# Kernel tuning notes

Hardware: AMD Instinct MI355X
Metric: run time of the kernel (lower is better)

The kernel has to match this reference:

```python
import jax, jax.numpy as jnp
import numpy as np

SHIFTS = [1, 3, 5, 7]
C = 16  # in_channels // 4
# -1 neighbor offsets for tmp1..tmp8 (dy, dx) in units of the dilation
OFFSETS = [(-1, -1), (-1, 0), (-1, 1), (0, 1), (1, 1), (1, 0), (1, -1), (0, -1)]


def setup_inputs() -> dict:
    key = jax.random.key(0)
    ks = jax.random.split(key, 32)
    d = {}
    d['cen'] = jax.random.normal(ks[0], (8, 64, 256, 256), jnp.float32)
    d['mas'] = jax.random.normal(ks[1], (8, 1, 256, 256), jnp.float32)
    d['in_conv_w'] = jax.random.normal(ks[2], (16, 64), jnp.float32) * 0.1
    d['in_conv_b'] = jax.random.normal(ks[3], (16,), jnp.float32) * 0.1
    for i, s in enumerate(SHIFTS):
        d[f'dw_w{s}'] = jax.random.normal(ks[4 + 2 * i], (16, 1, s, s), jnp.float32) * 0.1
        d[f'dw_b{s}'] = jax.random.normal(ks[5 + 2 * i], (16,), jnp.float32) * 0.1
    d['l1_w'] = jax.random.normal(ks[12], (4, 16, 4), jnp.float32) * 0.1
    d['l1_b'] = jax.random.normal(ks[13], (4, 16), jnp.float32) * 0.1
    d['l2_w'] = jax.random.normal(ks[14], (4, 16, 8), jnp.float32) * 0.1
    d['l2_b'] = jax.random.normal(ks[15], (4, 16), jnp.float32) * 0.1
    d['base_w'] = jax.random.normal(ks[16], (16, 4), jnp.float32) * 0.1
    d['bn_scale'] = jnp.ones((16,), jnp.float32)
    d['bn_bias'] = jnp.zeros((16,), jnp.float32)
    d['final_w'] = jax.random.normal(ks[17], (1, 16), jnp.float32) * 0.1
    d['final_b'] = jax.random.normal(ks[18], (1,), jnp.float32) * 0.1
    return d


def _dw_conv(x, w, b, pad):
    # depthwise conv, groups == channels
    y = jax.lax.conv_general_dilated(
        x, w, window_strides=(1, 1), padding=[(pad, pad), (pad, pad)],
        dimension_numbers=('NCHW', 'OIHW', 'NCHW'), feature_group_count=x.shape[1])
    return y + b[None, :, None, None]


def _shifted(x, dy, dx, d):
    # zero-padded shift: out(y,x) = in(y+dy, x+dx)
    H, W = x.shape[2], x.shape[3]
    p = jnp.pad(x, ((0, 0), (0, 0), (d, d), (d, d)))
    return p[:, :, d + dy:d + dy + H, d + dx:d + dx + W]


def _circ_shift(x, dw_w, dw_b, w1, b1, w2, b2, shift):
    x = _dw_conv(x, dw_w, dw_b, shift // 2)
    # tmp_k = x - x shifted by the k-th neighbor offset (dilation = shift)
    T = [x - _shifted(x, dy * shift, dx * shift, shift) for dy, dx in OFFSETS]
    # paired sums: S[k] = tmp_{k+1} + tmp_{k+5} (S repeats with period 4)
    S = [T[k] + T[k + 4] for k in range(4)]
    outs = []
    for k in range(8):  # fixed small structural loop
        feats = jnp.stack([S[(k + 1) % 4], S[(k + 3) % 4], S[(k + 2) % 4],
                           2.0 * T[(k + 4) % 8]], axis=2)  # (B,C,4,H,W)
        # grouped 1x1 conv (groups=C, 4C->C) == per-channel contraction over feature axis
        o = jnp.einsum('bcfhw,cf->bchw', feats, w1) + b1[None, :, None, None]
        outs.append(o * T[k])
    O = jnp.sort(jnp.stack(outs, axis=2), axis=2)  # (B,C,8,H,W) sorted over branch axis
    return jnp.einsum('bcfhw,cf->bchw', O, w2) + b2[None, :, None, None]


def reference(cen, mas, in_conv_w, in_conv_b, dw_w1, dw_b1, dw_w3, dw_b3,
              dw_w5, dw_b5, dw_w7, dw_b7, l1_w, l1_b, l2_w, l2_b,
              base_w, bn_scale, bn_bias, final_w, final_b):
    # in_conv: 1x1, in_channels -> C
    x = jnp.einsum('bihw,oi->bohw', cen, in_conv_w) + in_conv_b[None, :, None, None]
    dws = [(dw_w1, dw_b1), (dw_w3, dw_b3), (dw_w5, dw_b5), (dw_w7, dw_b7)]
    branches = [
        _circ_shift(x, dws[i][0], dws[i][1], l1_w[i], l1_b[i], l2_w[i], l2_b[i], SHIFTS[i])
        for i in range(len(SHIFTS))
    ]
    A = jnp.sort(jnp.stack(branches, axis=2), axis=2)  # (B,C,4,H,W)
    # out_conv: grouped 1x1 BaseConv (conv no-bias + BN(affine) + SiLU), then 1x1 -> 1, sigmoid
    y = jnp.einsum('bcfhw,cf->bchw', A, base_w)
    y = jax.nn.silu(y * bn_scale[None, :, None, None] + bn_bias[None, :, None, None])
    y = jnp.einsum('bchw,oc->bohw', y, final_w) + final_b[None, :, None, None]
    return jax.nn.sigmoid(y)
```

## Files before the change

kernel.cpp:

```cpp
#include <hip/hip_runtime.h>
#include <hip/hip_fp16.h>
#include <math.h>

#define HW 65536
#define PITCH 272
#define PLANE (PITCH * PITCH)

typedef float v2f __attribute__((ext_vector_type(2), aligned(8)));
typedef _Float16 h2 __attribute__((ext_vector_type(2)));

__device__ __forceinline__ h2 uh(unsigned u) { return __builtin_bit_cast(h2, u); }

#define CEH(a, b) { h2 _t = __builtin_elementwise_min(a, b); \
                    b = __builtin_elementwise_max(a, b); a = _t; }

__device__ __forceinline__ void sort8_h2(h2* v) {
    CEH(v[0], v[1]); CEH(v[2], v[3]); CEH(v[4], v[5]); CEH(v[6], v[7]);
    CEH(v[0], v[2]); CEH(v[1], v[3]); CEH(v[4], v[6]); CEH(v[5], v[7]);
    CEH(v[1], v[2]); CEH(v[5], v[6]); CEH(v[0], v[4]); CEH(v[3], v[7]);
    CEH(v[1], v[5]); CEH(v[2], v[6]);
    CEH(v[1], v[4]); CEH(v[3], v[6]);
    CEH(v[2], v[4]); CEH(v[3], v[5]);
    CEH(v[3], v[4]);
}
__device__ __forceinline__ void sort4_h2(h2* v) {
    CEH(v[0], v[1]); CEH(v[2], v[3]); CEH(v[0], v[2]); CEH(v[1], v[3]); CEH(v[1], v[2]);
}

__global__ __launch_bounds__(256) void k_pack(const float* __restrict__ l1w,
                                              const float* __restrict__ l1b,
                                              const float* __restrict__ l2w,
                                              const float* __restrict__ l2b,
                                              const float* __restrict__ bw,
                                              unsigned* __restrict__ wtab) {
    for (int t = threadIdx.x; t < 1088; t += 256) {
        float v = 0.f;
        if (t < 1024) {
            int c = t >> 6, i = (t >> 4) & 3, j = t & 15;
            if (j < 3)        v = l1w[i * 64 + c * 4 + j];
            else if (j == 3)  v = 2.f * l1w[i * 64 + c * 4 + 3];
            else if (j == 4)  v = l1b[i * 16 + c];
            else if (j < 13)  v = l2w[i * 128 + c * 8 + (j - 5)];
            else if (j == 13) v = l2b[i * 16 + c];
        } else {
            v = bw[t - 1024];
        }
        unsigned hs = (unsigned)__half_as_ushort(__float2half(v));
        wtab[t] = hs * 0x10001u;
    }
}

__global__ __launch_bounds__(256, 4) void k_inconv(const float* __restrict__ cen,
                                                   const float* __restrict__ w,
                                                   const float* __restrict__ bias,
                                                   __half* __restrict__ xh) {
    __shared__ float wl[1040];
    int tid = threadIdx.x;
    for (int t = tid; t < 1024; t += 256) wl[t] = w[(t & 15) * 64 + (t >> 4)];
    if (tid < 16) wl[1024 + tid] = bias[tid];
    __syncthreads();

    int q  = blockIdx.x * 256 + tid;
    int b_ = q >> 14;
    int hw = (q & 16383) * 4;
    const float* src = cen + (size_t)(b_ * 64) * HW + hw;

    float4 acc[16];
#pragma unroll
    for (int o = 0; o < 16; o++) { float bv = wl[1024 + o]; acc[o] = make_float4(bv, bv, bv, bv); }

#pragma unroll 4
    for (int i = 0; i < 64; i++) {
        float4 xv = *(const float4*)(src + (size_t)i * HW);
        const float4* wq = (const float4*)&wl[i * 16];
#pragma unroll
        for (int g = 0; g < 4; g++) {
            float4 f = wq[g];
            acc[g * 4 + 0].x += xv.x * f.x; acc[g * 4 + 0].y += xv.y * f.x;
            acc[g * 4 + 0].z += xv.z * f.x; acc[g * 4 + 0].w += xv.w * f.x;
            acc[g * 4 + 1].x += xv.x * f.y; acc[g * 4 + 1].y += xv.y * f.y;
            acc[g * 4 + 1].z += xv.z * f.y; acc[g * 4 + 1].w += xv.w * f.y;
            acc[g * 4 + 2].x += xv.x * f.z; acc[g * 4 + 2].y += xv.y * f.z;
            acc[g * 4 + 2].z += xv.z * f.z; acc[g * 4 + 2].w += xv.w * f.z;
            acc[g * 4 + 3].x += xv.x * f.w; acc[g * 4 + 3].y += xv.y * f.w;
            acc[g * 4 + 3].z += xv.z * f.w; acc[g * 4 + 3].w += xv.w * f.w;
        }
    }
    __half* dst = xh + (size_t)(b_ * 16) * HW + hw;
#pragma unroll
    for (int o = 0; o < 16; o++) {
        uint2 pk;
        pk.x = __builtin_bit_cast(unsigned, __floats2half2_rn(acc[o].x, acc[o].y));
        pk.y = __builtin_bit_cast(unsigned, __floats2half2_rn(acc[o].z, acc[o].w));
        *(uint2*)(dst + (size_t)o * HW) = pk;
    }
}

__global__ __launch_bounds__(256) void k_dw(const __half* __restrict__ xh,
    const float* __restrict__ dw_w1, const float* __restrict__ dw_b1,
    const float* __restrict__ dw_w3, const float* __restrict__ dw_b3,
    const float* __restrict__ dw_w5, const float* __restrict__ dw_b5,
    const float* __restrict__ dw_w7, const float* __restrict__ dw_b7,
    __half* __restrict__ conv) {
    const int plane = blockIdx.y;
    const int c     = plane & 15;
    const int P0    = (blockIdx.x >> 3) * 34;
    const int Q0    = (blockIdx.x & 7) * 34;
    const int tid   = threadIdx.x;

    __shared__ float lx[40 * 44];
    const __half* xp = xh + (size_t)plane * HW;

    for (int t = tid; t < 40 * 21; t += 256) {
        int r = t / 21, d = t - r * 21;
        int gy = P0 - 10 + r, gx = Q0 - 10 + 2 * d;
        float2 v = make_float2(0.f, 0.f);
        if ((unsigned)gy < 256u && (unsigned)gx < 256u)
            v = __half22float2(*(const __half2*)(xp + gy * 256 + gx));
        lx[r * 44 + 2 * d]     = v.x;
        lx[r * 44 + 2 * d + 1] = v.y;
    }
    __syncthreads();

    const float* W7 = dw_w7 + c * 49;
    const float* W5 = dw_w5 + c * 25;
    const float* W3 = dw_w3 + c * 9;
    const float  W1 = dw_w1[c];
    const float  B1 = dw_b1[c], B3 = dw_b3[c], B5 = dw_b5[c], B7 = dw_b7[c];

    for (int u = tid; u < 34 * 17; u += 256) {
        int row = u / 17;
        int pc0 = (u - row * 17) * 2;
        v2f c7v = {0, 0}, c5v = {0, 0}, c3v = {0, 0}, c1v = {0, 0};
#pragma unroll
        for (int a = 0; a < 7; a++) {
            const float* rp = &lx[(row + a) * 44 + pc0];
            v2f q0 = *(const v2f*)rp;
            v2f q1 = *(const v2f*)(rp + 2);
            v2f q2 = *(const v2f*)(rp + 4);
            v2f q3 = *(const v2f*)(rp + 6);
            float v8 = rp[8];
            float v[9] = {q0.x, q0.y, q1.x, q1.y, q2.x, q2.y, q3.x, q3.y, v8};
#pragma unroll
            for (int bb = 0; bb < 7; bb++) {
                v2f vv = {v[bb], v[bb + 1]};
                c7v += vv * W7[a * 7 + bb];
            }
            if (a >= 1 && a <= 5) {
#pragma unroll
                for (int bb = 0; bb < 5; bb++) {
                    v2f vv = {v[bb + 1], v[bb + 2]};
                    c5v += vv * W5[(a - 1) * 5 + bb];
                }
            }
            if (a >= 2 && a <= 4) {
#pragma unroll
                for (int bb = 0; bb < 3; bb++) {
                    v2f vv = {v[bb + 2], v[bb + 3]};
                    c3v += vv * W3[(a - 2) * 3 + bb];
                }
            }
            if (a == 3) {
                v2f vv = {v[3], v[4]};
                c1v = vv * W1;
            }
        }
        int py = P0 + row, px = Q0 + pc0;
        int iy = py - 7, ix = px - 7;
        bool rin = (unsigned)iy < 256u;
        bool in0 = rin && (unsigned)ix < 256u;
        bool in1 = rin && (unsigned)(ix + 1) < 256u;
        size_t o = (size_t)(plane * 4) * PLANE + (size_t)py * PITCH + px;
        *(__half2*)&conv[o]             = __floats2half2_rn(in0 ? c1v.x + B1 : 0.f, in1 ? c1v.y + B1 : 0.f);
        *(__half2*)&conv[o + PLANE]     = __floats2half2_rn(in0 ? c3v.x + B3 : 0.f, in1 ? c3v.y + B3 : 0.f);
        *(__half2*)&conv[o + 2 * PLANE] = __floats2half2_rn(in0 ? c5v.x + B5 : 0.f, in1 ? c5v.y + B5 : 0.f);
        *(__half2*)&conv[o + 3 * PLANE] = __floats2half2_rn(in0 ? c7v.x + B7 : 0.f, in1 ? c7v.y + B7 : 0.f);
    }
}

__global__ __launch_bounds__(512, 4) void k_mach(const __half* __restrict__ conv,
                                                 const unsigned* __restrict__ wtab,
                                                 const float* __restrict__ bns,
                                                 const float* __restrict__ bnb,
                                                 const float* __restrict__ fw,
                                                 const float* __restrict__ fb,
                                                 float* __restrict__ out) {
    const int b_  = blockIdx.y;
    const int ty0 = (blockIdx.x >> 3) * 32;
    const int tx0 = (blockIdx.x & 7) * 32;
    const int tid = threadIdx.x;
    const int py  = tid >> 4;
    const int pxp = tid & 15;

    __shared__ __align__(16) unsigned convt[4 * 46 * 24];

    float fyx = fb[0], fyy = fb[0];

    for (int c = 0; c < 16; c++) {
        if (c) __syncthreads();
        {
            const size_t pb4 = (size_t)(b_ * 64 + c * 4) * PLANE;
#pragma unroll
            for (int j = 0; j < 5; j++) {
                int t = tid + j * 512;
                if (t < 2208) {
                    int i  = t / 552;
                    int rm = t - i * 552;
                    int r  = rm / 12;
                    int d2 = rm - r * 12;
                    size_t E = pb4 + (size_t)i * PLANE + (size_t)(ty0 + r) * PITCH + tx0 + 4 * d2;
                    ((uint2*)convt)[t] = *(const uint2*)(conv + E);
                }
            }
        }
        __syncthreads();

        h2 bh[4];
#pragma unroll
        for (int i = 0; i < 4; i++) {
            const int s = 1 + 2 * i;
            const unsigned* pl = convt + i * 1104;
            const int q    = pxp + (7 - s) / 2;
            const int topb = (py + 7 - s) * 24 + q;
            const int midb = (py + 7) * 24 + q;
            const int botb = (py + 7 + s) * 24 + q;

            unsigned tt[8], tm[8], tb[8];
#pragma unroll
            for (int k = 0; k <= s; k++) {
                tt[k] = pl[topb + k];
                tm[k] = pl[midb + k];
                tb[k] = pl[botb + k];
            }
            const int m = s >> 1;
            h2 n0  = uh(tt[0]);
            h2 n1  = uh((tt[m] >> 16) | (tt[m + 1] << 16));
            h2 n2  = uh(tt[s]);
            h2 n7  = uh(tm[0]);
            h2 ctr = uh((tm[m] >> 16) | (tm[m + 1] << 16));
            h2 n3  = uh(tm[s]);
            h2 n6  = uh(tb[0]);
            h2 n5  = uh((tb[m] >> 16) | (tb[m + 1] << 16));
            h2 n4  = uh(tb[s]);

            h2 T[8];
            T[0] = ctr - n0; T[1] = ctr - n1; T[2] = ctr - n2; T[3] = ctr - n3;
            T[4] = ctr - n4; T[5] = ctr - n5; T[6] = ctr - n6; T[7] = ctr - n7;
            h2 S[4];
#pragma unroll
            for (int k = 0; k < 4; k++) S[k] = T[k] + T[k + 4];

            const unsigned* wt = wtab + ((c << 2) + i) * 16;
            h2 w10 = uh(wt[0]), w11 = uh(wt[1]), w12 = uh(wt[2]);
            h2 w13x2 = uh(wt[3]), bb1 = uh(wt[4]);

            h2 R[4];
#pragma unroll
            for (int mm = 0; mm < 4; mm++) {
                h2 r = S[(mm + 2) & 3] * w12 + bb1;
                r = S[(mm + 3) & 3] * w11 + r;
                r = S[(mm + 1) & 3] * w10 + r;
                R[mm] = r;
            }
            h2 h8[8];
#pragma unroll
            for (int k = 0; k < 8; k++)
                h8[k] = (T[(k + 4) & 7] * w13x2 + R[k & 3]) * T[k];
            sort8_h2(h8);

            h2 acc = uh(wt[13]);
#pragma unroll
            for (int k = 0; k < 8; k++) acc += h8[k] * uh(wt[5 + k]);
            bh[i] = acc;
        }
        sort4_h2(bh);
        h2 yv = bh[0] * uh(wtab[1024 + (c << 2)]);
#pragma unroll
        for (int k = 1; k < 4; k++) yv = bh[k] * uh(wtab[1024 + (c << 2) + k]) + yv;

        float zx = fmaf((float)yv.x, bns[c], bnb[c]);
        float zy = fmaf((float)yv.y, bns[c], bnb[c]);
        float sx = zx / (1.f + __expf(-zx));
        float sy = zy / (1.f + __expf(-zy));
        fyx = fmaf(sx, fw[c], fyx);
        fyy = fmaf(sy, fw[c], fyy);
    }
    float2 r;
    r.x = 1.f / (1.f + __expf(-fyx));
    r.y = 1.f / (1.f + __expf(-fyy));
    *(float2*)&out[((long)b_ << 16) + (ty0 + py) * 256 + tx0 + 2 * pxp] = r;
}

extern "C" void kernel_launch(void* const* d_in, const int* in_sizes, int n_in,
                              void* d_out, int out_size, void* d_ws, size_t ws_size,
                              hipStream_t stream) {
    (void)in_sizes; (void)n_in; (void)out_size; (void)ws_size;
    const float* cen   = (const float*)d_in[0];
    const float* in_w  = (const float*)d_in[2];
    const float* in_b  = (const float*)d_in[3];
    const float* dw_w1 = (const float*)d_in[4];
    const float* dw_b1 = (const float*)d_in[5];
    const float* dw_w3 = (const float*)d_in[6];
    const float* dw_b3 = (const float*)d_in[7];
    const float* dw_w5 = (const float*)d_in[8];
    const float* dw_b5 = (const float*)d_in[9];
    const float* dw_w7 = (const float*)d_in[10];
    const float* dw_b7 = (const float*)d_in[11];
    const float* l1w   = (const float*)d_in[12];
    const float* l1b   = (const float*)d_in[13];
    const float* l2w   = (const float*)d_in[14];
    const float* l2b   = (const float*)d_in[15];
    const float* bw    = (const float*)d_in[16];
    const float* bns   = (const float*)d_in[17];
    const float* bnb   = (const float*)d_in[18];
    const float* fw    = (const float*)d_in[19];
    const float* fb    = (const float*)d_in[20];

    __half*   xh   = (__half*)d_ws;
    __half*   conv = (__half*)((char*)d_ws + (size_t)16777216);
    unsigned* wtab = (unsigned*)((char*)d_ws + (size_t)16777216 + (size_t)75759616);
    float*    out  = (float*)d_out;

    k_pack<<<1, 256, 0, stream>>>(l1w, l1b, l2w, l2b, bw, wtab);
    k_inconv<<<512, 256, 0, stream>>>(cen, in_w, in_b, xh);
    k_dw<<<dim3(64, 128), 256, 0, stream>>>(xh, dw_w1, dw_b1, dw_w3, dw_b3,
                                            dw_w5, dw_b5, dw_w7, dw_b7, conv);
    k_mach<<<dim3(64, 8), 512, 0, stream>>>(conv, wtab, bns, bnb, fw, fb, out);
}
```

Before: 368.3 us.

## Split channel loop across blocks and add separate final reduction kernel

The mach kernel used to loop over all 16 channels inside each block, with 512 blocks in total. It now launches one block per (batch, channel) pair, 8192 blocks, and writes per-channel SiLU outputs as fp16 to a workspace buffer. A new k_final kernel reduces over the 16 channels with the final weights and applies the sigmoid. The aim is more parallelism and occupancy and no per-channel syncthreads loop, at the cost of an extra 16 MB round trip through global memory and one more launch. Shared-memory tile loads also widen from uint2 to uint4.

Result: no change. 364.8 us (-0.9%).

```diff
diff --git a/kernel.cpp b/kernel.cpp
--- a/kernel.cpp
+++ b/kernel.cpp
@@ -182,10 +182,9 @@
                                                  const unsigned* __restrict__ wtab,
                                                  const float* __restrict__ bns,
                                                  const float* __restrict__ bnb,
-                                                 const float* __restrict__ fw,
-                                                 const float* __restrict__ fb,
-                                                 float* __restrict__ out) {
-    const int b_  = blockIdx.y;
+                                                 __half* __restrict__ y16) {
+    const int by  = blockIdx.y;
+    const int c   = by & 15;
     const int ty0 = (blockIdx.x >> 3) * 32;
     const int tx0 = (blockIdx.x & 7) * 32;
     const int tid = threadIdx.x;
@@ -194,101 +193,117 @@
 
     __shared__ __align__(16) unsigned convt[4 * 46 * 24];
 
-    float fyx = fb[0], fyy = fb[0];
-
-    for (int c = 0; c < 16; c++) {
-        if (c) __syncthreads();
-        {
-            const size_t pb4 = (size_t)(b_ * 64 + c * 4) * PLANE;
-#pragma unroll
-            for (int j = 0; j < 5; j++) {
-                int t = tid + j * 512;
-                if (t < 2208) {
-                    int i  = t / 552;
-                    int rm = t - i * 552;
-                    int r  = rm / 12;
-                    int d2 = rm - r * 12;
-                    size_t E = pb4 + (size_t)i * PLANE + (size_t)(ty0 + r) * PITCH + tx0 + 4 * d2;
-                    ((uint2*)convt)[t] = *(const uint2*)(conv + E);
-                }
-            }
-        }
-        __syncthreads();
-
-        h2 bh[4];
-#pragma unroll
-        for (int i = 0; i < 4; i++) {
-            const int s = 1 + 2 * i;
-            const unsigned* pl = convt + i * 1104;
-            const int q    = pxp + (7 - s) / 2;
-            const int topb = (py + 7 - s) * 24 + q;
-            const int midb = (py + 7) * 24 + q;
-            const int botb = (py + 7 + s) * 24 + q;
-
-            unsigned tt[8], tm[8], tb[8];
-#pragma unroll
-            for (int k = 0; k <= s; k++) {
-                tt[k] = pl[topb + k];
-                tm[k] = pl[midb + k];
-                tb[k] = pl[botb + k];
-            }
-            const int m = s >> 1;
-            h2 n0  = uh(tt[0]);
-            h2 n1  = uh((tt[m] >> 16) | (tt[m + 1] << 16));
-            h2 n2  = uh(tt[s]);
-            h2 n7  = uh(tm[0]);
-            h2 ctr = uh((tm[m] >> 16) | (tm[m + 1] << 16));
-            h2 n3  = uh(tm[s]);
-            h2 n6  = uh(tb[0]);
-            h2 n5  = uh((tb[m] >> 16) | (tb[m + 1] << 16));
-            h2 n4  = uh(tb[s]);
-
-            h2 T[8];
-            T[0] = ctr - n0; T[1] = ctr - n1; T[2] = ctr - n2; T[3] = ctr - n3;
-            T[4] = ctr - n4; T[5] = ctr - n5; T[6] = ctr - n6; T[7] = ctr - n7;
-            h2 S[4];
-#pragma unroll
-            for (int k = 0; k < 4; k++) S[k] = T[k] + T[k + 4];
-
-            const unsigned* wt = wtab + ((c << 2) + i) * 16;
-            h2 w10 = uh(wt[0]), w11 = uh(wt[1]), w12 = uh(wt[2]);
-            h2 w13x2 = uh(wt[3]), bb1 = uh(wt[4]);
-
-            h2 R[4];
-#pragma unroll
-            for (int mm = 0; mm < 4; mm++) {
-                h2 r = S[(mm + 2) & 3] * w12 + bb1;
-                r = S[(mm + 3) & 3] * w11 + r;
-                r = S[(mm + 1) & 3] * w10 + r;
-                R[mm] = r;
-            }
-            h2 h8[8];
-#pragma unroll
-            for (int k = 0; k < 8; k++)
-                h8[k] = (T[(k + 4) & 7] * w13x2 + R[k & 3]) * T[k];
-            sort8_h2(h8);
-
-            h2 acc = uh(wt[13]);
-#pragma unroll
-            for (int k = 0; k < 8; k++) acc += h8[k] * uh(wt[5 + k]);
-            bh[i] = acc;
-        }
-        sort4_h2(bh);
-        h2 yv = bh[0] * uh(wtab[1024 + (c << 2)]);
-#pragma unroll
-        for (int k = 1; k < 4; k++) yv = bh[k] * uh(wtab[1024 + (c << 2) + k]) + yv;
-
-        float zx = fmaf((float)yv.x, bns[c], bnb[c]);
-        float zy = fmaf((float)yv.y, bns[c], bnb[c]);
-        float sx = zx / (1.f + __expf(-zx));
-        float sy = zy / (1.f + __expf(-zy));
-        fyx = fmaf(sx, fw[c], fyx);
-        fyy = fmaf(sy, fw[c], fyy);
+    {
+        const size_t pb4 = (size_t)(by * 4) * PLANE;
+#pragma unroll
+        for (int j = 0; j < 3; j++) {
+            int t = tid + j * 512;
+            if (t < 1104) {
+                int i  = t / 276;
+                int rm = t - i * 276;
+                int r  = rm / 6;
+                int d4 = rm - r * 6;
+                size_t E = pb4 + (size_t)i * PLANE + (size_t)(ty0 + r) * PITCH + tx0 + 8 * d4;
+                ((uint4*)convt)[t] = *(const uint4*)(conv + E);
+            }
+        }
+    }
+    __syncthreads();
+
+    h2 bh[4];
+#pragma unroll
+    for (int i = 0; i < 4; i++) {
+        const int s = 1 + 2 * i;
+        const unsigned* pl = convt + i * 1104;
+        const int q    = pxp + (7 - s) / 2;
+        const int topb = (py + 7 - s) * 24 + q;
+        const int midb = (py + 7) * 24 + q;
+        const int botb = (py + 7 + s) * 24 + q;
+
+        unsigned tt[8], tm[8], tb[8];
+#pragma unroll
+        for (int k = 0; k <= s; k++) {
+            tt[k] = pl[topb + k];
+            tm[k] = pl[midb + k];
+            tb[k] = pl[botb + k];
+        }
+        const int m = s >> 1;
+        h2 n0  = uh(tt[0]);
+        h2 n1  = uh((tt[m] >> 16) | (tt[m + 1] << 16));
+        h2 n2  = uh(tt[s]);
+        h2 n7  = uh(tm[0]);
+        h2 ctr = uh((tm[m] >> 16) | (tm[m + 1] << 16));
+        h2 n3  = uh(tm[s]);
+        h2 n6  = uh(tb[0]);
+        h2 n5  = uh((tb[m] >> 16) | (tb[m + 1] << 16));
+        h2 n4  = uh(tb[s]);
+
+        h2 T[8];
+        T[0] = ctr - n0; T[1] = ctr - n1; T[2] = ctr - n2; T[3] = ctr - n3;
+        T[4] = ctr - n4; T[5] = ctr - n5; T[6] = ctr - n6; T[7] = ctr - n7;
+        h2 S[4];
+#pragma unroll
+        for (int k = 0; k < 4; k++) S[k] = T[k] + T[k + 4];
+
+        const unsigned* wt = wtab + ((c << 2) + i) * 16;
+        h2 w10 = uh(wt[0]), w11 = uh(wt[1]), w12 = uh(wt[2]);
+        h2 w13x2 = uh(wt[3]), bb1 = uh(wt[4]);
+
+        h2 R[4];
+#pragma unroll
+        for (int mm = 0; mm < 4; mm++) {
+            h2 r = S[(mm + 2) & 3] * w12 + bb1;
+            r = S[(mm + 3) & 3] * w11 + r;
+            r = S[(mm + 1) & 3] * w10 + r;
+            R[mm] = r;
+        }
+        h2 h8[8];
+#pragma unroll
+        for (int k = 0; k < 8; k++)
+            h8[k] = (T[(k + 4) & 7] * w13x2 + R[k & 3]) * T[k];
+        sort8_h2(h8);
+
+        h2 acc = uh(wt[13]);
+#pragma unroll
+        for (int k = 0; k < 8; k++) acc += h8[k] * uh(wt[5 + k]);
+        bh[i] = acc;
+    }
+    sort4_h2(bh);
+    h2 yv = bh[0] * uh(wtab[1024 + (c << 2)]);
+#pragma unroll
+    for (int k = 1; k < 4; k++) yv = bh[k] * uh(wtab[1024 + (c << 2) + k]) + yv;
+
+    const float bsc = bns[c], bbi = bnb[c];
+    float zx = fmaf((float)yv.x, bsc, bbi);
+    float zy = fmaf((float)yv.y, bsc, bbi);
+    float sx = zx / (1.f + __expf(-zx));
+    float sy = zy / (1.f + __expf(-zy));
+    *(__half2*)&y16[(size_t)by * HW + (ty0 + py) * 256 + tx0 + 2 * pxp] =
+        __floats2half2_rn(sx, sy);
+}
+
+__global__ __launch_bounds__(256) void k_final(const __half* __restrict__ y16,
+                                               const float* __restrict__ fw,
+                                               const float* __restrict__ fb,
+                                               float* __restrict__ out) {
+    long t  = (long)blockIdx.x * 256 + threadIdx.x;
+    long p0 = t * 2;
+    int  b  = (int)(p0 >> 16);
+    int  hw = (int)(p0 & 65535);
+
+    float accx = fb[0], accy = fb[0];
+#pragma unroll
+    for (int cc = 0; cc < 16; cc++) {
+        __half2 h = *(const __half2*)(y16 + (size_t)(b * 16 + cc) * HW + hw);
+        float2 v = __half22float2(h);
+        float wv = fw[cc];
+        accx = fmaf(v.x, wv, accx);
+        accy = fmaf(v.y, wv, accy);
     }
     float2 r;
-    r.x = 1.f / (1.f + __expf(-fyx));
-    r.y = 1.f / (1.f + __expf(-fyy));
-    *(float2*)&out[((long)b_ << 16) + (ty0 + py) * 256 + tx0 + 2 * pxp] = r;
+    r.x = 1.f / (1.f + __expf(-accx));
+    r.y = 1.f / (1.f + __expf(-accy));
+    *(float2*)(out + p0) = r;
 }
 
 extern "C" void kernel_launch(void* const* d_in, const int* in_sizes, int n_in,
@@ -319,11 +334,13 @@
     __half*   xh   = (__half*)d_ws;
     __half*   conv = (__half*)((char*)d_ws + (size_t)16777216);
     unsigned* wtab = (unsigned*)((char*)d_ws + (size_t)16777216 + (size_t)75759616);
+    __half*   y16  = (__half*)((char*)d_ws + (size_t)16777216 + (size_t)75759616 + 8192);
     float*    out  = (float*)d_out;
 
     k_pack<<<1, 256, 0, stream>>>(l1w, l1b, l2w, l2b, bw, wtab);
     k_inconv<<<512, 256, 0, stream>>>(cen, in_w, in_b, xh);
     k_dw<<<dim3(64, 128), 256, 0, stream>>>(xh, dw_w1, dw_b1, dw_w3, dw_b3,
                                             dw_w5, dw_b5, dw_w7, dw_b7, conv);
-    k_mach<<<dim3(64, 8), 512, 0, stream>>>(conv, wtab, bns, bnb, fw, fb, out);
-}
+    k_mach<<<dim3(64, 128), 512, 0, stream>>>(conv, wtab, bns, bnb, y16);
+    k_final<<<1024, 256, 0, stream>>>(y16, fw, fb, out);
+}
```
